# Kernel optimization log

Hardware: AMD Instinct MI355X
Metric: run time of the kernel (lower is better)

The kernel has to match this reference:

```python
import jax, jax.numpy as jnp
import numpy as np

B, S, D, H = 2, 2048, 2048, 16
HD = D // H  # 128


def _rope_tables(seq_len, head_dim, base=10000.0):
    inv_freq = 1.0 / (base ** (np.arange(0, head_dim, 2, dtype=np.float32) / head_dim))
    t = np.arange(seq_len, dtype=np.float32)
    freqs = np.outer(t, inv_freq)  # [S, HD/2]
    return jnp.asarray(np.cos(freqs)), jnp.asarray(np.sin(freqs))


def setup_inputs() -> dict:
    key = jax.random.key(0)
    ks = jax.random.split(key, 5)
    std = 0.02
    inp = {
        "x": jax.random.normal(ks[0], (B, S, D), jnp.float32),
        "wq": jax.random.normal(ks[1], (D, D), jnp.float32) * std,
        "bq": jnp.zeros((D,), jnp.float32),
        "wk": jax.random.normal(ks[2], (D, D), jnp.float32) * std,
        "bk": jnp.zeros((D,), jnp.float32),
        "wv": jax.random.normal(ks[3], (D, D), jnp.float32) * std,
        "bv": jnp.zeros((D,), jnp.float32),
        "wo": jax.random.normal(ks[4], (D, D), jnp.float32) * std,
        "bo": jnp.zeros((D,), jnp.float32),
    }
    cos, sin = _rope_tables(S, HD)
    inp["freqs_cos"], inp["freqs_sin"] = cos, sin
    return inp


def _apply_rope(t, cos, sin):
    # t: [B,S,H,HD]; cos/sin: [S,HD/2] -> broadcast [1,S,1,HD/2]
    tp = t.reshape(*t.shape[:-1], HD // 2, 2)
    t1, t2 = tp[..., 0], tp[..., 1]
    c = cos[None, :, None, :]
    s = sin[None, :, None, :]
    out = jnp.stack([t1 * c - t2 * s, t1 * s + t2 * c], axis=-1)
    return out.reshape(t.shape)


def reference(x, wq, bq, wk, bk, wv, bv, wo, bo, freqs_cos, freqs_sin):
    b, s, d = x.shape
    q = (x @ wq.T + bq).reshape(b, s, H, HD)
    k = (x @ wk.T + bk).reshape(b, s, H, HD)
    v = (x @ wv.T + bv).reshape(b, s, H, HD)
    q = _apply_rope(q, freqs_cos, freqs_sin)
    k = _apply_rope(k, freqs_cos, freqs_sin)
    # causal SDPA: scores [B,H,S,S]
    scale = 1.0 / jnp.sqrt(jnp.asarray(HD, x.dtype))
    scores = jnp.einsum("bqhd,bkhd->bhqk", q, k) * scale
    causal = jnp.tril(jnp.ones((s, s), bool))
    scores = jnp.where(causal[None, None], scores, jnp.asarray(-1e30, scores.dtype))
    attn = jax.nn.softmax(scores.astype(jnp.float32), axis=-1).astype(x.dtype)
    out = jnp.einsum("bhqk,bkhd->bqhd", attn, v).reshape(b, s, d)
    return out @ wo.T + bo
```

## Files before the change

### kernel.cpp

```cpp
#include <hip/hip_runtime.h>


typedef __attribute__((ext_vector_type(8))) short short8;
typedef __attribute__((ext_vector_type(4))) float f32x4;
typedef __attribute__((ext_vector_type(16))) float f32x16;
typedef __attribute__((ext_vector_type(4))) unsigned short u16x4;
typedef __attribute__((ext_vector_type(8))) unsigned short u16x8;

constexpr int Bc = 2, Sc = 2048, Dc = 2048, Hc = 16, HDc = 128;
constexpr int Mc = Bc * Sc;
constexpr int Nc = Dc, Kc = Dc;

__device__ __forceinline__ unsigned short f2bf(float f) {
    union { float f; unsigned u; } x; x.f = f;
    unsigned r = x.u + 0x7FFFu + ((x.u >> 16) & 1u);
    return (unsigned short)(r >> 16);
}
__device__ __forceinline__ float bf2f(unsigned short u) {
    union { float f; unsigned u; } x; x.u = (unsigned)u << 16; return x.f;
}

__device__ __forceinline__ void g2lds16(const void* g, void* l) {
    __builtin_amdgcn_global_load_lds(
        (const __attribute__((address_space(1))) void*)g,
        (__attribute__((address_space(3))) void*)l, 16, 0, 0);
}

__global__ __launch_bounds__(256) void cvt_f32_bf16(
    const float* __restrict__ in, unsigned short* __restrict__ out, int n8) {
    int i = blockIdx.x * 256 + threadIdx.x;
    if (i >= n8) return;
    f32x4 a = *((const f32x4*)in + (size_t)i * 2);
    f32x4 b = *((const f32x4*)in + (size_t)i * 2 + 1);
    u16x8 o;
    o[0] = f2bf(a[0]); o[1] = f2bf(a[1]); o[2] = f2bf(a[2]); o[3] = f2bf(a[3]);
    o[4] = f2bf(b[0]); o[5] = f2bf(b[1]); o[6] = f2bf(b[2]); o[7] = f2bf(b[3]);
    *((u16x8*)out + i) = o;
}

template <int MODE>
__global__ __launch_bounds__(256) void gemm_nt(
    const unsigned short* __restrict__ A, const unsigned short* __restrict__ W,
    const float* __restrict__ bias, const float* __restrict__ rc,
    const float* __restrict__ rs, void* __restrict__ outp) {
    __shared__ __align__(16) unsigned short As[128 * 64];
    __shared__ __align__(16) unsigned short Bs[128 * 64];
    const int tid = threadIdx.x;
    const int w = tid >> 6, l = tid & 63;
    const int wm = w >> 1, wn = w & 1;
    const int lrow = l & 15, lhi = l >> 4;
    const int m0 = blockIdx.y * 128, n0 = blockIdx.x * 128;

    f32x4 acc[4][4];
#pragma unroll
    for (int i = 0; i < 4; ++i)
#pragma unroll
        for (int j = 0; j < 4; ++j) acc[i][j] = (f32x4){0.f, 0.f, 0.f, 0.f};

    for (int k0 = 0; k0 < Kc; k0 += 64) {
        __syncthreads();
#pragma unroll
        for (int i = 0; i < 4; ++i) {
            int s = i * 256 + tid;
            int row = s >> 3, c = s & 7;
            int cg = (c ^ (row & 7)) * 8;
            g2lds16(A + (size_t)(m0 + row) * Kc + k0 + cg,
                    &As[(size_t)(i * 256 + (w << 6)) * 8]);
            g2lds16(W + (size_t)(n0 + row) * Kc + k0 + cg,
                    &Bs[(size_t)(i * 256 + (w << 6)) * 8]);
        }
        __syncthreads();
#pragma unroll
        for (int kk = 0; kk < 2; ++kk) {
            short8 af[4], bf[4];
#pragma unroll
            for (int i = 0; i < 4; ++i) {
                int ra = wm * 64 + i * 16 + lrow;
                af[i] = *(const short8*)&As[ra * 64 + (((kk * 4 + lhi) ^ (ra & 7)) << 3)];
                int rb = wn * 64 + i * 16 + lrow;
                bf[i] = *(const short8*)&Bs[rb * 64 + (((kk * 4 + lhi) ^ (rb & 7)) << 3)];
            }
#pragma unroll
            for (int i = 0; i < 4; ++i)
#pragma unroll
                for (int j = 0; j < 4; ++j)
                    acc[i][j] = __builtin_amdgcn_mfma_f32_16x16x32_bf16(
                        af[i], bf[j], acc[i][j], 0, 0, 0);
        }
    }

#pragma unroll
    for (int i = 0; i < 4; ++i) {
#pragma unroll
        for (int j = 0; j < 4; ++j) {
            int gm0 = m0 + wm * 64 + i * 16 + lhi * 4;
            int gn  = n0 + wn * 64 + j * 16 + lrow;
            float bv = bias[gn];
            if (MODE == 0 || MODE == 1) {
                unsigned short* o = (unsigned short*)outp;
                int fi = (gn & (HDc - 1)) >> 1;
#pragma unroll
                for (int r = 0; r < 4; ++r) {
                    int gm = gm0 + r;
                    float v = acc[i][j][r] + bv;
                    float p = __shfl_xor(v, 1);
                    int pos = gm & (Sc - 1);
                    float cz = rc[pos * (HDc / 2) + fi];
                    float sz = rs[pos * (HDc / 2) + fi];
                    float ov = (gn & 1) ? (p * sz + v * cz) : (v * cz - p * sz);
                    o[(size_t)gm * Nc + gn] = f2bf(ov);
                }
            } else if (MODE == 2) {
                unsigned short* o = (unsigned short*)outp;
                int b = gm0 >> 11, sb = gm0 & (Sc - 1);
                u16x4 pk;
#pragma unroll
                for (int r = 0; r < 4; ++r) pk[r] = f2bf(acc[i][j][r] + bv);
                *(u16x4*)&o[((size_t)b * Dc + gn) * Sc + sb] = pk;
            } else {
                float* o = (float*)outp;
#pragma unroll
                for (int r = 0; r < 4; ++r)
                    o[(size_t)(gm0 + r) * Nc + gn] = acc[i][j][r] + bv;
            }
        }
    }
}

__global__ __launch_bounds__(256) void attn_fwd2(
    const unsigned short* __restrict__ Q, const unsigned short* __restrict__ Kb,
    const unsigned short* __restrict__ Vt, unsigned short* __restrict__ O) {
    __shared__ __align__(16) unsigned short Ks[2][64 * 128];
    __shared__ __align__(16) unsigned short Vs[2][128 * 64];
    const int tid = threadIdx.x;
    const int w = tid >> 6, l = tid & 63;
    const int ql = l & 31, H = l >> 5;
    const int pair = blockIdx.x;
    const int b = blockIdx.y >> 4, h = blockIdx.y & 15;
    const float SCL2 = 0.08838834764831845f * 1.4426950408889634f;

    const unsigned short* Kbase = Kb + ((size_t)b * Sc) * Dc + h * HDc;
    const unsigned short* Vbase = Vt + ((size_t)b * Dc + h * HDc) * Sc;

#define STAGE(tt, bb) {                                                        \
    const unsigned short* Kt = Kbase + (size_t)(tt) * 64 * Dc;                 \
    const unsigned short* Vp = Vbase + (tt) * 64;                              \
    _Pragma("unroll")                                                          \
    for (int i_ = 0; i_ < 4; ++i_) {                                           \
        int p_ = i_ * 256 + tid;                                               \
        int rK = p_ >> 4, sK = p_ & 15;                                        \
        g2lds16(Kt + (size_t)rK * Dc + ((sK ^ (rK & 15)) << 3),                \
                &Ks[bb][(i_ * 256 + (w << 6)) * 8]);                           \
        int rV = p_ >> 3, sV = p_ & 7;                                         \
        g2lds16(Vp + (size_t)rV * Sc + ((sV ^ (rV & 7)) << 3),                 \
                &Vs[bb][(i_ * 256 + (w << 6)) * 8]);                           \
    } }

#define PVSTEP(PC, HB, KS) {                                                   \
    int X0, X1, Y0, Y1;                                                        \
    asm("v_cvt_pk_bf16_f32 %0, %1, %2" : "=v"(X0) : "v"(PC[HB+0]), "v"(PC[HB+1])); \
    asm("v_cvt_pk_bf16_f32 %0, %1, %2" : "=v"(X1) : "v"(PC[HB+2]), "v"(PC[HB+3])); \
    asm("v_cvt_pk_bf16_f32 %0, %1, %2" : "=v"(Y0) : "v"(PC[HB+4]), "v"(PC[HB+5])); \
    asm("v_cvt_pk_bf16_f32 %0, %1, %2" : "=v"(Y1) : "v"(PC[HB+6]), "v"(PC[HB+7])); \
    asm("v_permlane32_swap_b32 %0, %1" : "+v"(X0), "+v"(Y0));                  \
    asm("v_permlane32_swap_b32 %0, %1" : "+v"(X1), "+v"(Y1));                  \
    union { int i[4]; short8 s; } pf_;                                         \
    pf_.i[0] = X0; pf_.i[1] = X1; pf_.i[2] = Y0; pf_.i[3] = Y1;                \
    _Pragma("unroll")                                                          \
    for (int dc_ = 0; dc_ < 4; ++dc_) {                                        \
        int rr = 32 * dc_ + ql;                                                \
        short8 vf = *(const short8*)&Vs[cur][rr * 64 + (((2*(KS)+H) ^ (rr & 7)) << 3)]; \
        accv[dc_] = __builtin_amdgcn_mfma_f32_32x32x16_bf16(vf, pf_.s, accv[dc_], 0, 0, 0); \
    } }

    for (int qi = 0; qi < 2; ++qi) {
        const int qt = qi ? (15 - pair) : pair;
        const int qb0 = qt * 128;
        const int qw0 = qb0 + w * 32;
        const int qg = qw0 + ql;

        short8 qf[8];
        {
            const unsigned short* qp = Q + ((size_t)(b * Sc + qg)) * Dc + h * HDc;
#pragma unroll
            for (int dc = 0; dc < 8; ++dc) {
                u16x8 v = *(const u16x8*)(qp + dc * 16 + H * 8);
                u16x8 o;
#pragma unroll
                for (int j = 0; j < 8; ++j) o[j] = f2bf(bf2f(v[j]) * SCL2);
                qf[dc] = (short8)o;
            }
        }
        f32x16 accv[4];
#pragma unroll
        for (int i = 0; i < 4; ++i) accv[i] = (f32x16)(0.f);
        float mrun = -3.0e38f, lrun = 0.f;
        const int nt = 2 * qt + 2;

        STAGE(0, 0);
        __syncthreads();
        int cur = 0;
        for (int t = 0; t < nt; ++t) {
            if (t + 1 < nt) STAGE(t + 1, cur ^ 1);
            const int kb0 = t * 64;
            if (kb0 <= qw0 + 31) {
                f32x16 a0 = (f32x16)(0.f), a1 = (f32x16)(0.f);
#pragma unroll
                for (int dc = 0; dc < 8; ++dc) {
                    int r0 = ql, r1 = 32 + ql, sl = dc * 2 + H;
                    short8 k0 = *(const short8*)&Ks[cur][r0 * 128 + ((sl ^ (r0 & 15)) << 3)];
                    short8 k1 = *(const short8*)&Ks[cur][r1 * 128 + ((sl ^ (r1 & 15)) << 3)];
                    a0 = __builtin_amdgcn_mfma_f32_32x32x16_bf16(k0, qf[dc], a0, 0, 0, 0);
                    a1 = __builtin_amdgcn_mfma_f32_32x32x16_bf16(k1, qf[dc], a1, 0, 0, 0);
                }
                if (t >= 2 * qt) {
#pragma unroll
                    for (int r = 0; r < 16; ++r) {
                        int kl = (r & 3) + 8 * (r >> 2) + 4 * H;
                        if (kb0 + kl > qg)      a0[r] = -3.0e38f;
                        if (kb0 + 32 + kl > qg) a1[r] = -3.0e38f;
                    }
                }
                float pm = -3.0e38f;
#pragma unroll
                for (int r = 0; r < 16; ++r) pm = fmaxf(pm, a0[r]);
#pragma unroll
                for (int r = 0; r < 16; ++r) pm = fmaxf(pm, a1[r]);
                pm = fmaxf(pm, __shfl_xor(pm, 32));
                float mnew = fmaxf(mrun, pm);
                float fs = exp2f(mrun - mnew);
                float p0[16], p1[16], ps = 0.f;
#pragma unroll
                for (int r = 0; r < 16; ++r) { p0[r] = exp2f(a0[r] - mnew); ps += p0[r]; }
#pragma unroll
                for (int r = 0; r < 16; ++r) { p1[r] = exp2f(a1[r] - mnew); ps += p1[r]; }
                ps += __shfl_xor(ps, 32);
                mrun = mnew;
                lrun = lrun * fs + ps;
#pragma unroll
                for (int dc = 0; dc < 4; ++dc)
#pragma unroll
                    for (int r = 0; r < 16; ++r) accv[dc][r] *= fs;
                PVSTEP(p0, 0, 0); PVSTEP(p0, 8, 1);
                PVSTEP(p1, 0, 2); PVSTEP(p1, 8, 3);
            }
            __syncthreads();
            cur ^= 1;
        }
        float inv = 1.f / lrun;
        unsigned short* Op = O + ((size_t)(b * Sc + qg)) * Dc + h * HDc;
#pragma unroll
        for (int dc = 0; dc < 4; ++dc)
#pragma unroll
            for (int rg = 0; rg < 4; ++rg) {
                int d0 = 32 * dc + 8 * rg + 4 * H;
                u16x4 pk;
#pragma unroll
                for (int j = 0; j < 4; ++j) pk[j] = f2bf(accv[dc][rg * 4 + j] * inv);
                *(u16x4*)(Op + d0) = pk;
            }
    }
#undef STAGE
#undef PVSTEP
}

extern "C" void kernel_launch(void* const* d_in, const int* in_sizes, int n_in,
                              void* d_out, int out_size, void* d_ws, size_t ws_size,
                              hipStream_t stream) {
    const float* x  = (const float*)d_in[0];
    const float* wq = (const float*)d_in[1];
    const float* bq = (const float*)d_in[2];
    const float* wk = (const float*)d_in[3];
    const float* bk = (const float*)d_in[4];
    const float* wv = (const float*)d_in[5];
    const float* bv = (const float*)d_in[6];
    const float* wo = (const float*)d_in[7];
    const float* bo = (const float*)d_in[8];
    const float* rc = (const float*)d_in[9];
    const float* rs = (const float*)d_in[10];

    const size_t NE = (size_t)Mc * Dc;
    const size_t NW = (size_t)Dc * Dc;

    unsigned short* xb = (unsigned short*)d_ws;
    unsigned short* qb = xb + NE;
    unsigned short* kb = qb + NE;
    unsigned short* vt = kb + NE;
    unsigned short* wb = vt + NE;

    const int ne8 = (int)(NE / 8), nw8 = (int)(NW / 8);
    dim3 gg(Nc / 128, Mc / 128), tb(256);

    cvt_f32_bf16<<<dim3(ne8 / 256), tb, 0, stream>>>(x, xb, ne8);

    cvt_f32_bf16<<<dim3(nw8 / 256), tb, 0, stream>>>(wq, wb, nw8);
    gemm_nt<0><<<gg, tb, 0, stream>>>(xb, wb, bq, rc, rs, qb);

    cvt_f32_bf16<<<dim3(nw8 / 256), tb, 0, stream>>>(wk, wb, nw8);
    gemm_nt<1><<<gg, tb, 0, stream>>>(xb, wb, bk, rc, rs, kb);

    cvt_f32_bf16<<<dim3(nw8 / 256), tb, 0, stream>>>(wv, wb, nw8);
    gemm_nt<2><<<gg, tb, 0, stream>>>(xb, wb, bv, rc, rs, vt);

    attn_fwd2<<<dim3(8, Bc * Hc), tb, 0, stream>>>(qb, kb, vt, xb);

    cvt_f32_bf16<<<dim3(nw8 / 256), tb, 0, stream>>>(wo, wb, nw8);
    gemm_nt<3><<<gg, tb, 0, stream>>>(xb, wb, bo, rc, rs, d_out);
}
```

Before: 300.7 us.

## Triple-buffer attention K/V, lazy softmax rescale, fold Q scale, batch conversions

Attention now uses three K/V LDS buffers with explicit vmcnt waits and raw barriers, so loads for tile t+2 overlap compute. It also raises wave priority around the MFMA sections and skips the accumulator rescale unless the running max grows by more than 8. The softmax scale is folded into the Q projection epilogue, which removes the per-load rescale in attention. When the workspace is large enough, all five f32-to-bf16 conversions run in one batched launch into separate weight buffers. The grid axes are swapped. Costs are more LDS per block, which may lower occupancy, and a deferred-max softmax that relies on fp32 headroom.

```diff
diff --git a/kernel.cpp b/kernel.cpp
--- a/kernel.cpp
+++ b/kernel.cpp
@@ -10,15 +10,13 @@
 constexpr int Bc = 2, Sc = 2048, Dc = 2048, Hc = 16, HDc = 128;
 constexpr int Mc = Bc * Sc;
 constexpr int Nc = Dc, Kc = Dc;
+constexpr float QSCL = 0.08838834764831845f * 1.4426950408889634f;
 
 __device__ __forceinline__ unsigned short f2bf(float f) {
     union { float f; unsigned u; } x; x.f = f;
     unsigned r = x.u + 0x7FFFu + ((x.u >> 16) & 1u);
     return (unsigned short)(r >> 16);
 }
-__device__ __forceinline__ float bf2f(unsigned short u) {
-    union { float f; unsigned u; } x; x.u = (unsigned)u << 16; return x.f;
-}
 
 __device__ __forceinline__ void g2lds16(const void* g, void* l) {
     __builtin_amdgcn_global_load_lds(
@@ -26,16 +24,39 @@
         (__attribute__((address_space(3))) void*)l, 16, 0, 0);
 }
 
-__global__ __launch_bounds__(256) void cvt_f32_bf16(
-    const float* __restrict__ in, unsigned short* __restrict__ out, int n8) {
-    int i = blockIdx.x * 256 + threadIdx.x;
-    if (i >= n8) return;
+__device__ __forceinline__ void cvt_body(const float* __restrict__ in,
+                                         unsigned short* __restrict__ out, int i) {
     f32x4 a = *((const f32x4*)in + (size_t)i * 2);
     f32x4 b = *((const f32x4*)in + (size_t)i * 2 + 1);
     u16x8 o;
     o[0] = f2bf(a[0]); o[1] = f2bf(a[1]); o[2] = f2bf(a[2]); o[3] = f2bf(a[3]);
     o[4] = f2bf(b[0]); o[5] = f2bf(b[1]); o[6] = f2bf(b[2]); o[7] = f2bf(b[3]);
     *((u16x8*)out + i) = o;
+}
+
+__global__ __launch_bounds__(256) void cvt_f32_bf16(
+    const float* __restrict__ in, unsigned short* __restrict__ out, int n8) {
+    int i = blockIdx.x * 256 + threadIdx.x;
+    if (i >= n8) return;
+    cvt_body(in, out, i);
+}
+
+__global__ __launch_bounds__(256) void cvt_batch(
+    const float* __restrict__ x,  unsigned short* __restrict__ xo,
+    const float* __restrict__ w0, unsigned short* __restrict__ o0,
+    const float* __restrict__ w1, unsigned short* __restrict__ o1,
+    const float* __restrict__ w2, unsigned short* __restrict__ o2,
+    const float* __restrict__ w3, unsigned short* __restrict__ o3) {
+    const int which = blockIdx.y;
+    const float* in; unsigned short* out; int n8;
+    if (which == 0)      { in = x;  out = xo; n8 = (Mc * Dc) / 8; }
+    else if (which == 1) { in = w0; out = o0; n8 = (Dc * Dc) / 8; }
+    else if (which == 2) { in = w1; out = o1; n8 = (Dc * Dc) / 8; }
+    else if (which == 3) { in = w2; out = o2; n8 = (Dc * Dc) / 8; }
+    else                 { in = w3; out = o3; n8 = (Dc * Dc) / 8; }
+    int i = blockIdx.x * 256 + threadIdx.x;
+    if (i >= n8) return;
+    cvt_body(in, out, i);
 }
 
 template <int MODE>
@@ -108,6 +129,7 @@
                     float cz = rc[pos * (HDc / 2) + fi];
                     float sz = rs[pos * (HDc / 2) + fi];
                     float ov = (gn & 1) ? (p * sz + v * cz) : (v * cz - p * sz);
+                    if (MODE == 0) ov *= QSCL;
                     o[(size_t)gm * Nc + gn] = f2bf(ov);
                 }
             } else if (MODE == 2) {
@@ -127,22 +149,22 @@
     }
 }
 
-__global__ __launch_bounds__(256) void attn_fwd2(
+__global__ __launch_bounds__(256) void attn_fwd3(
     const unsigned short* __restrict__ Q, const unsigned short* __restrict__ Kb,
     const unsigned short* __restrict__ Vt, unsigned short* __restrict__ O) {
-    __shared__ __align__(16) unsigned short Ks[2][64 * 128];
-    __shared__ __align__(16) unsigned short Vs[2][128 * 64];
+    __shared__ __align__(16) unsigned short Ks[3][64 * 128];
+    __shared__ __align__(16) unsigned short Vs[3][128 * 64];
     const int tid = threadIdx.x;
     const int w = tid >> 6, l = tid & 63;
-    const int ql = l & 31, H = l >> 5;
-    const int pair = blockIdx.x;
-    const int b = blockIdx.y >> 4, h = blockIdx.y & 15;
-    const float SCL2 = 0.08838834764831845f * 1.4426950408889634f;
+    const int ql = l & 31, Hh = l >> 5;
+    const int bh = blockIdx.x;
+    const int pair = blockIdx.y;
+    const int b = bh >> 4, h = bh & 15;
 
     const unsigned short* Kbase = Kb + ((size_t)b * Sc) * Dc + h * HDc;
     const unsigned short* Vbase = Vt + ((size_t)b * Dc + h * HDc) * Sc;
 
-#define STAGE(tt, bb) {                                                        \
+#define STAGE(tt, kd, vd) {                                                    \
     const unsigned short* Kt = Kbase + (size_t)(tt) * 64 * Dc;                 \
     const unsigned short* Vp = Vbase + (tt) * 64;                              \
     _Pragma("unroll")                                                          \
@@ -150,10 +172,10 @@
         int p_ = i_ * 256 + tid;                                               \
         int rK = p_ >> 4, sK = p_ & 15;                                        \
         g2lds16(Kt + (size_t)rK * Dc + ((sK ^ (rK & 15)) << 3),                \
-                &Ks[bb][(i_ * 256 + (w << 6)) * 8]);                           \
+                (kd) + (i_ * 256 + (w << 6)) * 8);                             \
         int rV = p_ >> 3, sV = p_ & 7;                                         \
         g2lds16(Vp + (size_t)rV * Sc + ((sV ^ (rV & 7)) << 3),                 \
-                &Vs[bb][(i_ * 256 + (w << 6)) * 8]);                           \
+                (vd) + (i_ * 256 + (w << 6)) * 8);                             \
     } }
 
 #define PVSTEP(PC, HB, KS) {                                                   \
@@ -169,27 +191,21 @@
     _Pragma("unroll")                                                          \
     for (int dc_ = 0; dc_ < 4; ++dc_) {                                        \
         int rr = 32 * dc_ + ql;                                                \
-        short8 vf = *(const short8*)&Vs[cur][rr * 64 + (((2*(KS)+H) ^ (rr & 7)) << 3)]; \
+        short8 vf = *(const short8*)&Vbuf[rr * 64 + (((2*(KS)+Hh) ^ (rr & 7)) << 3)]; \
         accv[dc_] = __builtin_amdgcn_mfma_f32_32x32x16_bf16(vf, pf_.s, accv[dc_], 0, 0, 0); \
     } }
 
     for (int qi = 0; qi < 2; ++qi) {
         const int qt = qi ? (15 - pair) : pair;
-        const int qb0 = qt * 128;
-        const int qw0 = qb0 + w * 32;
+        const int qw0 = qt * 128 + w * 32;
         const int qg = qw0 + ql;
 
         short8 qf[8];
         {
             const unsigned short* qp = Q + ((size_t)(b * Sc + qg)) * Dc + h * HDc;
 #pragma unroll
-            for (int dc = 0; dc < 8; ++dc) {
-                u16x8 v = *(const u16x8*)(qp + dc * 16 + H * 8);
-                u16x8 o;
-#pragma unroll
-                for (int j = 0; j < 8; ++j) o[j] = f2bf(bf2f(v[j]) * SCL2);
-                qf[dc] = (short8)o;
-            }
+            for (int dc = 0; dc < 8; ++dc)
+                qf[dc] = *(const short8*)(qp + dc * 16 + Hh * 8);
         }
         f32x16 accv[4];
 #pragma unroll
@@ -197,26 +213,38 @@
         float mrun = -3.0e38f, lrun = 0.f;
         const int nt = 2 * qt + 2;
 
-        STAGE(0, 0);
-        __syncthreads();
-        int cur = 0;
+        STAGE(0, Ks[0], Vs[0]);
+        STAGE(1, Ks[1], Vs[1]);
         for (int t = 0; t < nt; ++t) {
-            if (t + 1 < nt) STAGE(t + 1, cur ^ 1);
+            if (t + 2 < nt) {
+                STAGE(t + 2, Ks[(t + 2) % 3], Vs[(t + 2) % 3]);
+                asm volatile("s_waitcnt vmcnt(16)" ::: "memory");
+            } else if (t + 1 < nt) {
+                asm volatile("s_waitcnt vmcnt(8)" ::: "memory");
+            } else {
+                asm volatile("s_waitcnt vmcnt(0)" ::: "memory");
+            }
+            __builtin_amdgcn_s_barrier();
+
+            const unsigned short* Kbuf = Ks[t % 3];
+            const unsigned short* Vbuf = Vs[t % 3];
             const int kb0 = t * 64;
             if (kb0 <= qw0 + 31) {
                 f32x16 a0 = (f32x16)(0.f), a1 = (f32x16)(0.f);
+                __builtin_amdgcn_s_setprio(1);
 #pragma unroll
                 for (int dc = 0; dc < 8; ++dc) {
-                    int r0 = ql, r1 = 32 + ql, sl = dc * 2 + H;
-                    short8 k0 = *(const short8*)&Ks[cur][r0 * 128 + ((sl ^ (r0 & 15)) << 3)];
-                    short8 k1 = *(const short8*)&Ks[cur][r1 * 128 + ((sl ^ (r1 & 15)) << 3)];
+                    int r0 = ql, r1 = 32 + ql, sl = dc * 2 + Hh;
+                    short8 k0 = *(const short8*)&Kbuf[r0 * 128 + ((sl ^ (r0 & 15)) << 3)];
+                    short8 k1 = *(const short8*)&Kbuf[r1 * 128 + ((sl ^ (r1 & 15)) << 3)];
                     a0 = __builtin_amdgcn_mfma_f32_32x32x16_bf16(k0, qf[dc], a0, 0, 0, 0);
                     a1 = __builtin_amdgcn_mfma_f32_32x32x16_bf16(k1, qf[dc], a1, 0, 0, 0);
                 }
+                __builtin_amdgcn_s_setprio(0);
                 if (t >= 2 * qt) {
 #pragma unroll
                     for (int r = 0; r < 16; ++r) {
-                        int kl = (r & 3) + 8 * (r >> 2) + 4 * H;
+                        int kl = (r & 3) + 8 * (r >> 2) + 4 * Hh;
                         if (kb0 + kl > qg)      a0[r] = -3.0e38f;
                         if (kb0 + 32 + kl > qg) a1[r] = -3.0e38f;
                     }
@@ -227,25 +255,29 @@
 #pragma unroll
                 for (int r = 0; r < 16; ++r) pm = fmaxf(pm, a1[r]);
                 pm = fmaxf(pm, __shfl_xor(pm, 32));
-                float mnew = fmaxf(mrun, pm);
-                float fs = exp2f(mrun - mnew);
+                if (!__all(pm - mrun <= 8.0f)) {
+                    float mnew = fmaxf(mrun, pm);
+                    float fs = exp2f(mrun - mnew);
+                    mrun = mnew;
+                    lrun *= fs;
+#pragma unroll
+                    for (int dc = 0; dc < 4; ++dc)
+#pragma unroll
+                        for (int r = 0; r < 16; ++r) accv[dc][r] *= fs;
+                }
                 float p0[16], p1[16], ps = 0.f;
 #pragma unroll
-                for (int r = 0; r < 16; ++r) { p0[r] = exp2f(a0[r] - mnew); ps += p0[r]; }
-#pragma unroll
-                for (int r = 0; r < 16; ++r) { p1[r] = exp2f(a1[r] - mnew); ps += p1[r]; }
+                for (int r = 0; r < 16; ++r) { p0[r] = exp2f(a0[r] - mrun); ps += p0[r]; }
+#pragma unroll
+                for (int r = 0; r < 16; ++r) { p1[r] = exp2f(a1[r] - mrun); ps += p1[r]; }
                 ps += __shfl_xor(ps, 32);
-                mrun = mnew;
-                lrun = lrun * fs + ps;
-#pragma unroll
-                for (int dc = 0; dc < 4; ++dc)
-#pragma unroll
-                    for (int r = 0; r < 16; ++r) accv[dc][r] *= fs;
+                lrun += ps;
+                __builtin_amdgcn_s_setprio(1);
                 PVSTEP(p0, 0, 0); PVSTEP(p0, 8, 1);
                 PVSTEP(p1, 0, 2); PVSTEP(p1, 8, 3);
-            }
-            __syncthreads();
-            cur ^= 1;
+                __builtin_amdgcn_s_setprio(0);
+            }
+            __builtin_amdgcn_s_barrier();
         }
         float inv = 1.f / lrun;
         unsigned short* Op = O + ((size_t)(b * Sc + qg)) * Dc + h * HDc;
@@ -253,7 +285,7 @@
         for (int dc = 0; dc < 4; ++dc)
 #pragma unroll
             for (int rg = 0; rg < 4; ++rg) {
-                int d0 = 32 * dc + 8 * rg + 4 * H;
+                int d0 = 32 * dc + 8 * rg + 4 * Hh;
                 u16x4 pk;
 #pragma unroll
                 for (int j = 0; j < 4; ++j) pk[j] = f2bf(accv[dc][rg * 4 + j] * inv);
@@ -290,20 +322,30 @@
 
     const int ne8 = (int)(NE / 8), nw8 = (int)(NW / 8);
     dim3 gg(Nc / 128, Mc / 128), tb(256);
-
-    cvt_f32_bf16<<<dim3(ne8 / 256), tb, 0, stream>>>(x, xb, ne8);
-
-    cvt_f32_bf16<<<dim3(nw8 / 256), tb, 0, stream>>>(wq, wb, nw8);
-    gemm_nt<0><<<gg, tb, 0, stream>>>(xb, wb, bq, rc, rs, qb);
-
-    cvt_f32_bf16<<<dim3(nw8 / 256), tb, 0, stream>>>(wk, wb, nw8);
-    gemm_nt<1><<<gg, tb, 0, stream>>>(xb, wb, bk, rc, rs, kb);
-
-    cvt_f32_bf16<<<dim3(nw8 / 256), tb, 0, stream>>>(wv, wb, nw8);
-    gemm_nt<2><<<gg, tb, 0, stream>>>(xb, wb, bv, rc, rs, vt);
-
-    attn_fwd2<<<dim3(8, Bc * Hc), tb, 0, stream>>>(qb, kb, vt, xb);
-
-    cvt_f32_bf16<<<dim3(nw8 / 256), tb, 0, stream>>>(wo, wb, nw8);
-    gemm_nt<3><<<gg, tb, 0, stream>>>(xb, wb, bo, rc, rs, d_out);
-}
+    const bool big_ws = ws_size >= (4 * NE + 4 * NW) * sizeof(unsigned short);
+
+    if (big_ws) {
+        unsigned short* wqb = wb;
+        unsigned short* wkb = wb + NW;
+        unsigned short* wvb = wb + 2 * NW;
+        unsigned short* wob = wb + 3 * NW;
+        cvt_batch<<<dim3(ne8 / 256, 5), tb, 0, stream>>>(
+            x, xb, wq, wqb, wk, wkb, wv, wvb, wo, wob);
+        gemm_nt<0><<<gg, tb, 0, stream>>>(xb, wqb, bq, rc, rs, qb);
+        gemm_nt<1><<<gg, tb, 0, stream>>>(xb, wkb, bk, rc, rs, kb);
+        gemm_nt<2><<<gg, tb, 0, stream>>>(xb, wvb, bv, rc, rs, vt);
+        attn_fwd3<<<dim3(Bc * Hc, 8), tb, 0, stream>>>(qb, kb, vt, xb);
+        gemm_nt<3><<<gg, tb, 0, stream>>>(xb, wob, bo, rc, rs, d_out);
+    } else {
+        cvt_f32_bf16<<<dim3(ne8 / 256), tb, 0, stream>>>(x, xb, ne8);
+        cvt_f32_bf16<<<dim3(nw8 / 256), tb, 0, stream>>>(wq, wb, nw8);
+        gemm_nt<0><<<gg, tb, 0, stream>>>(xb, wb, bq, rc, rs, qb);
+        cvt_f32_bf16<<<dim3(nw8 / 256), tb, 0, stream>>>(wk, wb, nw8);
+        gemm_nt<1><<<gg, tb, 0, stream>>>(xb, wb, bk, rc, rs, kb);
+        cvt_f32_bf16<<<dim3(nw8 / 256), tb, 0, stream>>>(wv, wb, nw8);
+        gemm_nt<2><<<gg, tb, 0, stream>>>(xb, wb, bv, rc, rs, vt);
+        attn_fwd3<<<dim3(Bc * Hc, 8), tb, 0, stream>>>(qb, kb, vt, xb);
+        cvt_f32_bf16<<<dim3(nw8 / 256), tb, 0, stream>>>(wo, wb, nw8);
+        gemm_nt<3><<<gg, tb, 0, stream>>>(xb, wb, bo, rc, rs, d_out);
+    }
+}
```

After: 281.8 us. -6.3%, faster.
